# Optimization experiments

Hardware: AMD Instinct MI355X
Metric: run time of the kernel (lower is better)

The kernel has to match this reference:

```python
import jax, jax.numpy as jnp
import numpy as np

NUM_CLUSTERS = 64
KMEANS_ITERS = 10
EPS = 1e-8


def _pairwise_sqdist(a, b):
    # a: [n, d], b: [k, d] -> [n, k] squared euclidean distances
    a2 = jnp.sum(a * a, axis=-1, keepdims=True)          # [n, 1]
    b2 = jnp.sum(b * b, axis=-1)                          # [k]
    d2 = a2 - 2.0 * (a @ b.T) + b2[None, :]
    return jnp.maximum(d2, 0.0)


def _kmeans(data, num_clusters, iters=KMEANS_ITERS):
    # Lloyd's algorithm with deterministic init (first K points),
    # standing in for sklearn KMeans.fit (fixed iteration count for jit).
    centers0 = data[:num_clusters]                        # [K, d]

    def step(centers, _):
        d2 = _pairwise_sqdist(data, centers)              # [n, K]
        assign = jnp.argmin(d2, axis=-1)                  # [n]
        sums = jax.ops.segment_sum(data, assign, num_segments=num_clusters)
        counts = jax.ops.segment_sum(jnp.ones((data.shape[0],), data.dtype),
                                     assign, num_segments=num_clusters)
        new_centers = jnp.where(counts[:, None] > 0,
                                sums / jnp.maximum(counts[:, None], 1.0),
                                centers)
        return new_centers, None

    centers, _ = jax.lax.scan(step, centers0, None, length=iters)
    return centers


def setup_inputs() -> dict:
    key = jax.random.key(0)
    x = jax.random.normal(key, (16, 2048, 512), dtype=jnp.float32)
    return {"x": x}


def reference(x):
    B, N, d = x.shape
    data = x.reshape(B * N, d)                            # [n, d]
    # KMeans runs on detached data in the original (CPU sklearn) -> no grad.
    centers = jax.lax.stop_gradient(_kmeans(data, NUM_CLUSTERS))  # [K, d]
    dist = jnp.sqrt(_pairwise_sqdist(data, centers))      # [n, K]
    inv = 1.0 / (dist + EPS)                              # pairwise inverse euclidean distance
    return inv.reshape(B, N, NUM_CLUSTERS)
```

## Files before the change

### kernel.cpp

```cpp
#include <hip/hip_runtime.h>
#include <math.h>

#define N_PTS 32768
#define DIM   512
#define K_CL  64
#define ITERS 10
#define EPS_F 1e-8f

typedef __attribute__((ext_vector_type(8))) short          short8v;
typedef __attribute__((ext_vector_type(8))) unsigned short ushort8v;
typedef __attribute__((ext_vector_type(4))) float          f32x4v;

__device__ __forceinline__ unsigned short f2bf(float f) {
    unsigned u = __builtin_bit_cast(unsigned, f);
    unsigned r = u + 0x7fffu + ((u >> 16) & 1u);
    return (unsigned short)(r >> 16);
}
__device__ __forceinline__ float bf2f(unsigned short h) {
    return __builtin_bit_cast(float, ((unsigned)h) << 16);
}


__global__ void init_centers(const float* __restrict__ x,
                             float* __restrict__ ct,
                             float* __restrict__ c2,
                             unsigned short* __restrict__ cth,
                             unsigned short* __restrict__ ctl) {
    int k = blockIdx.x;
    int t = threadIdx.x;
    float ssum = 0.f;
    for (int d = t; d < DIM; d += 256) {
        float v = x[k * DIM + d];
        ct[d * K_CL + k] = v;
        unsigned short h = f2bf(v);
        cth[k * DIM + d] = h;
        ctl[k * DIM + d] = f2bf(v - bf2f(h));
        ssum += v * v;
    }
    #pragma unroll
    for (int off = 32; off; off >>= 1) ssum += __shfl_down(ssum, off);
    __shared__ float red[4];
    if ((t & 63) == 0) red[t >> 6] = ssum;
    __syncthreads();
    if (t == 0) c2[k] = red[0] + red[1] + red[2] + red[3];
}

__launch_bounds__(64)
__global__ void assign_mfma(const float* __restrict__ x,
                            const unsigned short* __restrict__ cth,
                            const unsigned short* __restrict__ ctl,
                            const float* __restrict__ c2,
                            int* __restrict__ assignv) {
    const int lane  = threadIdx.x;
    const int mbase = blockIdx.x * 16;
    const int mrow  = lane & 15;
    const int kgrp  = lane >> 4;

    const float* xr = x + (size_t)(mbase + mrow) * DIM + kgrp * 8;
    const unsigned short* cbh = cth + (size_t)mrow * DIM + kgrp * 8;
    const unsigned short* cbl = ctl + (size_t)mrow * DIM + kgrp * 8;

    f32x4v acc[4];
    acc[0] = acc[1] = acc[2] = acc[3] = (f32x4v){0.f, 0.f, 0.f, 0.f};

    float4 xraw[2][2];
    xraw[0][0] = *(const float4*)(xr);
    xraw[0][1] = *(const float4*)(xr + 4);

    int buf = 0;
    for (int ks = 0; ks < 16; ++ks) {
        if (ks < 15) {
            xraw[buf ^ 1][0] = *(const float4*)(xr + (ks + 1) * 32);
            xraw[buf ^ 1][1] = *(const float4*)(xr + (ks + 1) * 32 + 4);
        }
        short8v bh[4], bl[4];
        #pragma unroll
        for (int nt = 0; nt < 4; ++nt) {
            const size_t off = (size_t)nt * 16 * DIM + ks * 32;
            bh[nt] = *(const short8v*)(cbh + off);
            bl[nt] = *(const short8v*)(cbl + off);
        }
        short8v ah, al;
        {
            float fs[8] = {xraw[buf][0].x, xraw[buf][0].y,
                           xraw[buf][0].z, xraw[buf][0].w,
                           xraw[buf][1].x, xraw[buf][1].y,
                           xraw[buf][1].z, xraw[buf][1].w};
            ushort8v h, l;
            #pragma unroll
            for (int i = 0; i < 8; ++i) {
                unsigned short hh = f2bf(fs[i]);
                h[i] = hh;
                l[i] = f2bf(fs[i] - bf2f(hh));
            }
            ah = __builtin_bit_cast(short8v, h);
            al = __builtin_bit_cast(short8v, l);
        }
        #pragma unroll
        for (int nt = 0; nt < 4; ++nt) {
            acc[nt] = __builtin_amdgcn_mfma_f32_16x16x32_bf16(
                ah, bh[nt], acc[nt], 0, 0, 0);
            acc[nt] = __builtin_amdgcn_mfma_f32_16x16x32_bf16(
                ah, bl[nt], acc[nt], 0, 0, 0);
            acc[nt] = __builtin_amdgcn_mfma_f32_16x16x32_bf16(
                al, bh[nt], acc[nt], 0, 0, 0);
        }
        buf ^= 1;
    }

    float c2v[4];
    #pragma unroll
    for (int nt = 0; nt < 4; ++nt) c2v[nt] = c2[nt * 16 + mrow];

    #pragma unroll
    for (int r = 0; r < 4; ++r) {
        float bv = 1e30f; int bc = 0;
        #pragma unroll
        for (int nt = 0; nt < 4; ++nt) {
            float v = c2v[nt] - 2.0f * acc[nt][r];
            if (v < bv) { bv = v; bc = nt * 16 + mrow; }
        }
        #pragma unroll
        for (int m = 1; m < 16; m <<= 1) {
            float ov = __shfl_xor(bv, m);
            int   oc = __shfl_xor(bc, m);
            if (ov < bv || (ov == bv && oc < bc)) { bv = ov; bc = oc; }
        }
        if (mrow == 0) assignv[mbase + kgrp * 4 + r] = bc;
    }
}

__launch_bounds__(512)
__global__ void build_gather(const float* __restrict__ x,
                             const int* __restrict__ assignv,
                             int* __restrict__ rcnt,
                             float* __restrict__ part) {
    const int k    = blockIdx.x;
    const int pc   = blockIdx.y;
    const int t    = threadIdx.x;
    const int lane = t & 63;
    const int w    = t >> 6;
    const int p0   = pc * 4096;

    __shared__ int                lst[4096];
    __shared__ unsigned long long msk[64];
    __shared__ int                cnt[64];
    __shared__ int                basel[64];
    __shared__ int                ntot;

    #pragma unroll
    for (int j = 0; j < 8; ++j) {
        const int chunk = w * 8 + j;
        const int a = assignv[p0 + chunk * 64 + lane];
        unsigned long long m = __ballot(a == k);
        if (lane == 0) { msk[chunk] = m; cnt[chunk] = __popcll(m); }
    }
    __syncthreads();

    if (w == 0) {
        const int v = cnt[lane];
        int incl = v;
        #pragma unroll
        for (int off = 1; off < 64; off <<= 1) {
            int u = __shfl_up(incl, off);
            if (lane >= off) incl += u;
        }
        basel[lane] = incl - v;
        if (lane == 63) { ntot = incl; rcnt[k * 8 + pc] = incl; }
    }
    __syncthreads();

    #pragma unroll
    for (int j = 0; j < 8; ++j) {
        const int chunk = w * 8 + j;
        const unsigned long long m = msk[chunk];
        if ((m >> lane) & 1ull) {
            const int pos = basel[chunk] +
                __popcll(m & ((1ull << lane) - 1ull));
            lst[pos] = p0 + chunk * 64 + lane;
        }
    }
    __syncthreads();

    const int n = ntot;
    float acc = 0.f;
    int s = 0;
    for (; s + 8 <= n; s += 8) {
        int idx[8];
        #pragma unroll
        for (int q = 0; q < 8; ++q) idx[q] = lst[s + q];
        #pragma unroll
        for (int q = 0; q < 8; ++q) acc += x[(size_t)idx[q] * DIM + t];
    }
    for (; s < n; ++s) acc += x[(size_t)lst[s] * DIM + t];
    part[((size_t)k * 8 + pc) * DIM + t] = acc;
}

__global__ void update_centers(float* __restrict__ ct,
                               const float* __restrict__ part,
                               const int* __restrict__ rcnt,
                               float* __restrict__ c2,
                               unsigned short* __restrict__ cth,
                               unsigned short* __restrict__ ctl) {
    int k = blockIdx.x;
    int t = threadIdx.x;
    int cnt = 0;
    #pragma unroll
    for (int pc = 0; pc < 8; ++pc) cnt += rcnt[k * 8 + pc];
    float fc = (float)cnt;
    float ssum = 0.f;
    for (int d = t; d < DIM; d += 256) {
        float v = ct[d * K_CL + k];
        if (cnt > 0) {
            float s = 0.f;
            #pragma unroll
            for (int pc = 0; pc < 8; ++pc)
                s += part[((size_t)k * 8 + pc) * DIM + d];
            v = s / fc;
        }
        ct[d * K_CL + k] = v;
        unsigned short h = f2bf(v);
        cth[k * DIM + d] = h;
        ctl[k * DIM + d] = f2bf(v - bf2f(h));
        ssum += v * v;
    }
    #pragma unroll
    for (int off = 32; off; off >>= 1) ssum += __shfl_down(ssum, off);
    __shared__ float red[4];
    if ((t & 63) == 0) red[t >> 6] = ssum;
    __syncthreads();
    if (t == 0) c2[k] = red[0] + red[1] + red[2] + red[3];
}

#define DMA_T(tt, bb)                                                          \
    {                                                                          \
        _Pragma("unroll")                                                      \
        for (int q_ = 0; q_ < 4; ++q_) {                                       \
            __builtin_amdgcn_global_load_lds(                                  \
                (const __attribute__((address_space(1))) void*)                \
                    (ct + (tt) * 2048 + q_ * 512 + tid * 4),                   \
                (__attribute__((address_space(3))) void*)                      \
                    (&cs[bb][q_ * 512 + tid * 4]),                             \
                16, 0, 0);                                                     \
        }                                                                      \
        {                                                                      \
            const int row_ = tid >> 3;                                         \
            const int kq_  = (tid & 7) ^ ((row_ >> 1) & 7);                    \
            __builtin_amdgcn_global_load_lds(                                  \
                (const __attribute__((address_space(1))) void*)                \
                    (x + (size_t)(pbase + row_) * DIM +                        \
                     (tt) * 32 + kq_ * 4),                                     \
                (__attribute__((address_space(3))) void*)                      \
                    (&xs[bb][tid * 4]),                                        \
                16, 0, 0);                                                     \
        }                                                                      \
    }

#define LOADX(sl, kq)                                                          \
    {                                                                          \
        _Pragma("unroll")                                                      \
        for (int i_ = 0; i_ < 2; ++i_) {                                       \
            const int row_ = rr * 2 + i_;                                      \
            xv[sl][i_] = *(const float4*)(                                     \
                &xs[buf][(row_ * 8 + ((kq) ^ (row_ >> 1))) * 4]);              \
        }                                                                      \
    }

#define LOADC(sl, kq)                                                          \
    {                                                                          \
        _Pragma("unroll")                                                      \
        for (int j_ = 0; j_ < 4; ++j_)                                         \
            cv[sl][j_] = *(const float4*)(&cs[buf][((kq) * 4 + j_) * 64 +      \
                                                   c * 4]);                    \
    }

#define BODY_DIST(kq)                                                          \
    {                                                                          \
        if ((kq) < 7) { LOADX(((kq) + 1) & 1, (kq) + 1);                       \
                        LOADC(((kq) + 1) & 1, (kq) + 1); }                     \
        const float4 c0 = cv[(kq) & 1][0], c1 = cv[(kq) & 1][1];               \
        const float4 c2v = cv[(kq) & 1][2], c3 = cv[(kq) & 1][3];              \
        _Pragma("unroll")                                                      \
        for (int i = 0; i < 2; ++i) {                                          \
            const float4 xq = xv[(kq) & 1][i];                                 \
            float d0, d1, d2, d3;                                              \
            d0 = xq.x - c0.x;  acc[i][0] += d0 * d0;                           \
            d1 = xq.x - c0.y;  acc[i][1] += d1 * d1;                           \
            d2 = xq.x - c0.z;  acc[i][2] += d2 * d2;                           \
            d3 = xq.x - c0.w;  acc[i][3] += d3 * d3;                           \
            d0 = xq.y - c1.x;  acc[i][0] += d0 * d0;                           \
            d1 = xq.y - c1.y;  acc[i][1] += d1 * d1;                           \
            d2 = xq.y - c1.z;  acc[i][2] += d2 * d2;                           \
            d3 = xq.y - c1.w;  acc[i][3] += d3 * d3;                           \
            d0 = xq.z - c2v.x; acc[i][0] += d0 * d0;                           \
            d1 = xq.z - c2v.y; acc[i][1] += d1 * d1;                           \
            d2 = xq.z - c2v.z; acc[i][2] += d2 * d2;                           \
            d3 = xq.z - c2v.w; acc[i][3] += d3 * d3;                           \
            d0 = xq.w - c3.x;  acc[i][0] += d0 * d0;                           \
            d1 = xq.w - c3.y;  acc[i][1] += d1 * d1;                           \
            d2 = xq.w - c3.z;  acc[i][2] += d2 * d2;                           \
            d3 = xq.w - c3.w;  acc[i][3] += d3 * d3;                           \
        }                                                                      \
    }

__launch_bounds__(128, 4)
__global__ void final_dist(const float* __restrict__ x,
                           const float* __restrict__ ct,
                           float* __restrict__ out) {
    __shared__ float xs[2][512];
    __shared__ float cs[2][2048];

    const int tid = threadIdx.x;
    const int pbase = blockIdx.x * 16;
    const int rr = tid >> 4;
    const int c  = tid & 15;

    float4 xv[2][2];
    float4 cv[2][4];
    float acc[2][4] = {};

    DMA_T(0, 0);
    __syncthreads();

    int buf = 0;
    for (int t = 0; t < 16; ++t) {
        if (t < 15) DMA_T(t + 1, buf ^ 1);
        LOADX(0, 0); LOADC(0, 0);
        BODY_DIST(0); BODY_DIST(1); BODY_DIST(2); BODY_DIST(3);
        BODY_DIST(4); BODY_DIST(5); BODY_DIST(6); BODY_DIST(7);
        __syncthreads();
        buf ^= 1;
    }

    #pragma unroll
    for (int i = 0; i < 2; ++i) {
        int p = pbase + rr * 2 + i;
        float4 o;
        o.x = 1.0f / (sqrtf(acc[i][0]) + EPS_F);
        o.y = 1.0f / (sqrtf(acc[i][1]) + EPS_F);
        o.z = 1.0f / (sqrtf(acc[i][2]) + EPS_F);
        o.w = 1.0f / (sqrtf(acc[i][3]) + EPS_F);
        *(float4*)(out + (size_t)p * K_CL + c * 4) = o;
    }
}

extern "C" void kernel_launch(void* const* d_in, const int* in_sizes, int n_in,
                              void* d_out, int out_size, void* d_ws, size_t ws_size,
                              hipStream_t stream) {
    (void)in_sizes; (void)n_in; (void)out_size; (void)ws_size;
    const float* x = (const float*)d_in[0];
    float* ws      = (float*)d_ws;
    float* ct      = ws;
    float* c2      = ws + 65536;
    unsigned short* cth = (unsigned short*)(ws + 65600);
    unsigned short* ctl = (unsigned short*)(ws + 81984);
    int*   rcnt    = (int*)(ws + 98368);
    int*   assignv = (int*)(ws + 98880);
    float* part    = ws + 131648;
    float* out     = (float*)d_out;

    init_centers<<<64, 256, 0, stream>>>(x, ct, c2, cth, ctl);
    for (int it = 0; it < ITERS; ++it) {
        assign_mfma<<<2048, 64, 0, stream>>>(x, cth, ctl, c2, assignv);
        build_gather<<<dim3(64, 8), 512, 0, stream>>>(x, assignv, rcnt, part);
        update_centers<<<64, 256, 0, stream>>>(ct, part, rcnt, c2, cth, ctl);
    }
    final_dist<<<2048, 128, 0, stream>>>(x, ct, out);
}
```

Measured before the change: 761.1 us.

## Double row tiles in assign and final kernels, prefetch centers, unroll gather loop

The assign kernel now processes 32 points per wave instead of 16. It reuses each loaded center fragment across two MFMA row tiles and double-buffers both the center and point loads. The gather loop gets a 32-wide unrolled path so more independent global loads are in flight at once. The final distance kernel moves to 256-thread blocks covering 32 points, with matching changes to the DMA split, the LDS x buffer size and the swizzle mask. Together these trade more registers and shared memory per block for fewer center reloads and fewer blocks, which may reduce occupancy.

```diff
diff --git a/kernel.cpp b/kernel.cpp
--- a/kernel.cpp
+++ b/kernel.cpp
@@ -45,6 +45,74 @@
     if (t == 0) c2[k] = red[0] + red[1] + red[2] + red[3];
 }
 
+__device__ __forceinline__ void splitx(const float4 a, const float4 b,
+                                       short8v& ah, short8v& al) {
+    float fs[8] = {a.x, a.y, a.z, a.w, b.x, b.y, b.z, b.w};
+    ushort8v h, l;
+    #pragma unroll
+    for (int i = 0; i < 8; ++i) {
+        unsigned short hh = f2bf(fs[i]);
+        h[i] = hh;
+        l[i] = f2bf(fs[i] - bf2f(hh));
+    }
+    ah = __builtin_bit_cast(short8v, h);
+    al = __builtin_bit_cast(short8v, l);
+}
+
+#define ASTEP(ks_, CUR, NXT)                                                   \
+    {                                                                          \
+        if ((ks_) < 15) {                                                      \
+            _Pragma("unroll")                                                  \
+            for (int nt = 0; nt < 4; ++nt) {                                   \
+                const size_t off = (size_t)nt * 16 * DIM + ((ks_) + 1) * 32;   \
+                bh[NXT][nt] = *(const short8v*)(cbh + off);                    \
+                bl[NXT][nt] = *(const short8v*)(cbl + off);                    \
+            }                                                                  \
+            xr0v[NXT][0] = *(const float4*)(xr0 + ((ks_) + 1) * 32);           \
+            xr0v[NXT][1] = *(const float4*)(xr0 + ((ks_) + 1) * 32 + 4);       \
+            xr1v[NXT][0] = *(const float4*)(xr1 + ((ks_) + 1) * 32);           \
+            xr1v[NXT][1] = *(const float4*)(xr1 + ((ks_) + 1) * 32 + 4);       \
+        }                                                                      \
+        short8v ah0, al0, ah1, al1;                                            \
+        splitx(xr0v[CUR][0], xr0v[CUR][1], ah0, al0);                          \
+        splitx(xr1v[CUR][0], xr1v[CUR][1], ah1, al1);                          \
+        _Pragma("unroll")                                                      \
+        for (int nt = 0; nt < 4; ++nt) {                                       \
+            acc0[nt] = __builtin_amdgcn_mfma_f32_16x16x32_bf16(                \
+                ah0, bh[CUR][nt], acc0[nt], 0, 0, 0);                          \
+            acc0[nt] = __builtin_amdgcn_mfma_f32_16x16x32_bf16(                \
+                ah0, bl[CUR][nt], acc0[nt], 0, 0, 0);                          \
+            acc0[nt] = __builtin_amdgcn_mfma_f32_16x16x32_bf16(                \
+                al0, bh[CUR][nt], acc0[nt], 0, 0, 0);                          \
+            acc1[nt] = __builtin_amdgcn_mfma_f32_16x16x32_bf16(                \
+                ah1, bh[CUR][nt], acc1[nt], 0, 0, 0);                          \
+            acc1[nt] = __builtin_amdgcn_mfma_f32_16x16x32_bf16(                \
+                ah1, bl[CUR][nt], acc1[nt], 0, 0, 0);                          \
+            acc1[nt] = __builtin_amdgcn_mfma_f32_16x16x32_bf16(                \
+                al1, bh[CUR][nt], acc1[nt], 0, 0, 0);                          \
+        }                                                                      \
+    }
+
+#define ARGMIN_WRITE(ACC, PB)                                                  \
+    {                                                                          \
+        _Pragma("unroll")                                                      \
+        for (int r = 0; r < 4; ++r) {                                          \
+            float bv = 1e30f; int bc = 0;                                      \
+            _Pragma("unroll")                                                  \
+            for (int nt = 0; nt < 4; ++nt) {                                   \
+                float v = c2v[nt] - 2.0f * ACC[nt][r];                         \
+                if (v < bv) { bv = v; bc = nt * 16 + mrow; }                   \
+            }                                                                  \
+            _Pragma("unroll")                                                  \
+            for (int m = 1; m < 16; m <<= 1) {                                 \
+                float ov = __shfl_xor(bv, m);                                  \
+                int   oc = __shfl_xor(bc, m);                                  \
+                if (ov < bv || (ov == bv && oc < bc)) { bv = ov; bc = oc; }    \
+            }                                                                  \
+            if (mrow == 0) assignv[(PB) + kgrp * 4 + r] = bc;                  \
+        }                                                                      \
+    }
+
 __launch_bounds__(64)
 __global__ void assign_mfma(const float* __restrict__ x,
                             const unsigned short* __restrict__ cth,
@@ -52,82 +120,47 @@
                             const float* __restrict__ c2,
                             int* __restrict__ assignv) {
     const int lane  = threadIdx.x;
-    const int mbase = blockIdx.x * 16;
+    const int mbase = blockIdx.x * 32;
     const int mrow  = lane & 15;
     const int kgrp  = lane >> 4;
 
-    const float* xr = x + (size_t)(mbase + mrow) * DIM + kgrp * 8;
+    const float* xr0 = x + (size_t)(mbase + mrow) * DIM + kgrp * 8;
+    const float* xr1 = x + (size_t)(mbase + 16 + mrow) * DIM + kgrp * 8;
     const unsigned short* cbh = cth + (size_t)mrow * DIM + kgrp * 8;
     const unsigned short* cbl = ctl + (size_t)mrow * DIM + kgrp * 8;
 
-    f32x4v acc[4];
-    acc[0] = acc[1] = acc[2] = acc[3] = (f32x4v){0.f, 0.f, 0.f, 0.f};
-
-    float4 xraw[2][2];
-    xraw[0][0] = *(const float4*)(xr);
-    xraw[0][1] = *(const float4*)(xr + 4);
-
-    int buf = 0;
-    for (int ks = 0; ks < 16; ++ks) {
-        if (ks < 15) {
-            xraw[buf ^ 1][0] = *(const float4*)(xr + (ks + 1) * 32);
-            xraw[buf ^ 1][1] = *(const float4*)(xr + (ks + 1) * 32 + 4);
-        }
-        short8v bh[4], bl[4];
-        #pragma unroll
-        for (int nt = 0; nt < 4; ++nt) {
-            const size_t off = (size_t)nt * 16 * DIM + ks * 32;
-            bh[nt] = *(const short8v*)(cbh + off);
-            bl[nt] = *(const short8v*)(cbl + off);
-        }
-        short8v ah, al;
-        {
-            float fs[8] = {xraw[buf][0].x, xraw[buf][0].y,
-                           xraw[buf][0].z, xraw[buf][0].w,
-                           xraw[buf][1].x, xraw[buf][1].y,
-                           xraw[buf][1].z, xraw[buf][1].w};
-            ushort8v h, l;
-            #pragma unroll
-            for (int i = 0; i < 8; ++i) {
-                unsigned short hh = f2bf(fs[i]);
-                h[i] = hh;
-                l[i] = f2bf(fs[i] - bf2f(hh));
-            }
-            ah = __builtin_bit_cast(short8v, h);
-            al = __builtin_bit_cast(short8v, l);
-        }
-        #pragma unroll
-        for (int nt = 0; nt < 4; ++nt) {
-            acc[nt] = __builtin_amdgcn_mfma_f32_16x16x32_bf16(
-                ah, bh[nt], acc[nt], 0, 0, 0);
-            acc[nt] = __builtin_amdgcn_mfma_f32_16x16x32_bf16(
-                ah, bl[nt], acc[nt], 0, 0, 0);
-            acc[nt] = __builtin_amdgcn_mfma_f32_16x16x32_bf16(
-                al, bh[nt], acc[nt], 0, 0, 0);
-        }
-        buf ^= 1;
+    f32x4v acc0[4], acc1[4];
+    #pragma unroll
+    for (int nt = 0; nt < 4; ++nt) {
+        acc0[nt] = (f32x4v){0.f, 0.f, 0.f, 0.f};
+        acc1[nt] = (f32x4v){0.f, 0.f, 0.f, 0.f};
+    }
+
+    short8v bh[2][4], bl[2][4];
+    float4  xr0v[2][2], xr1v[2][2];
+
+    #pragma unroll
+    for (int nt = 0; nt < 4; ++nt) {
+        const size_t off = (size_t)nt * 16 * DIM;
+        bh[0][nt] = *(const short8v*)(cbh + off);
+        bl[0][nt] = *(const short8v*)(cbl + off);
+    }
+    xr0v[0][0] = *(const float4*)(xr0);
+    xr0v[0][1] = *(const float4*)(xr0 + 4);
+    xr1v[0][0] = *(const float4*)(xr1);
+    xr1v[0][1] = *(const float4*)(xr1 + 4);
+
+    for (int kp = 0; kp < 8; ++kp) {
+        ASTEP(2 * kp,     0, 1)
+        ASTEP(2 * kp + 1, 1, 0)
     }
 
     float c2v[4];
     #pragma unroll
     for (int nt = 0; nt < 4; ++nt) c2v[nt] = c2[nt * 16 + mrow];
 
-    #pragma unroll
-    for (int r = 0; r < 4; ++r) {
-        float bv = 1e30f; int bc = 0;
-        #pragma unroll
-        for (int nt = 0; nt < 4; ++nt) {
-            float v = c2v[nt] - 2.0f * acc[nt][r];
-            if (v < bv) { bv = v; bc = nt * 16 + mrow; }
-        }
-        #pragma unroll
-        for (int m = 1; m < 16; m <<= 1) {
-            float ov = __shfl_xor(bv, m);
-            int   oc = __shfl_xor(bc, m);
-            if (ov < bv || (ov == bv && oc < bc)) { bv = ov; bc = oc; }
-        }
-        if (mrow == 0) assignv[mbase + kgrp * 4 + r] = bc;
-    }
+    ARGMIN_WRITE(acc0, mbase)
+    ARGMIN_WRITE(acc1, mbase + 16)
 }
 
 __launch_bounds__(512)
@@ -185,6 +218,16 @@
     const int n = ntot;
     float acc = 0.f;
     int s = 0;
+    for (; s + 32 <= n; s += 32) {
+        int idx[32];
+        #pragma unroll
+        for (int q = 0; q < 32; ++q) idx[q] = lst[s + q];
+        float v[32];
+        #pragma unroll
+        for (int q = 0; q < 32; ++q) v[q] = x[(size_t)idx[q] * DIM + t];
+        #pragma unroll
+        for (int q = 0; q < 32; ++q) acc += v[q];
+    }
     for (; s + 8 <= n; s += 8) {
         int idx[8];
         #pragma unroll
@@ -235,12 +278,12 @@
 #define DMA_T(tt, bb)                                                          \
     {                                                                          \
         _Pragma("unroll")                                                      \
-        for (int q_ = 0; q_ < 4; ++q_) {                                       \
+        for (int q_ = 0; q_ < 2; ++q_) {                                       \
             __builtin_amdgcn_global_load_lds(                                  \
                 (const __attribute__((address_space(1))) void*)                \
-                    (ct + (tt) * 2048 + q_ * 512 + tid * 4),                   \
+                    (ct + (tt) * 2048 + q_ * 1024 + tid * 4),                  \
                 (__attribute__((address_space(3))) void*)                      \
-                    (&cs[bb][q_ * 512 + tid * 4]),                             \
+                    (&cs[bb][q_ * 1024 + tid * 4]),                            \
                 16, 0, 0);                                                     \
         }                                                                      \
         {                                                                      \
@@ -262,7 +305,7 @@
         for (int i_ = 0; i_ < 2; ++i_) {                                       \
             const int row_ = rr * 2 + i_;                                      \
             xv[sl][i_] = *(const float4*)(                                     \
-                &xs[buf][(row_ * 8 + ((kq) ^ (row_ >> 1))) * 4]);              \
+                &xs[buf][(row_ * 8 + ((kq) ^ ((row_ >> 1) & 7))) * 4]);        \
         }                                                                      \
     }
 
@@ -303,15 +346,15 @@
         }                                                                      \
     }
 
-__launch_bounds__(128, 4)
+__launch_bounds__(256, 6)
 __global__ void final_dist(const float* __restrict__ x,
                            const float* __restrict__ ct,
                            float* __restrict__ out) {
-    __shared__ float xs[2][512];
+    __shared__ float xs[2][1024];
     __shared__ float cs[2][2048];
 
     const int tid = threadIdx.x;
-    const int pbase = blockIdx.x * 16;
+    const int pbase = blockIdx.x * 32;
     const int rr = tid >> 4;
     const int c  = tid & 15;
 
@@ -361,9 +404,9 @@
 
     init_centers<<<64, 256, 0, stream>>>(x, ct, c2, cth, ctl);
     for (int it = 0; it < ITERS; ++it) {
-        assign_mfma<<<2048, 64, 0, stream>>>(x, cth, ctl, c2, assignv);
+        assign_mfma<<<1024, 64, 0, stream>>>(x, cth, ctl, c2, assignv);
         build_gather<<<dim3(64, 8), 512, 0, stream>>>(x, assignv, rcnt, part);
         update_centers<<<64, 256, 0, stream>>>(ct, part, rcnt, c2, cth, ctl);
     }
-    final_dist<<<2048, 128, 0, stream>>>(x, ct, out);
-}
+    final_dist<<<1024, 256, 0, stream>>>(x, ct, out);
+}
```

Result: slower. 800.6 us (+5.2%).
